# Performance work log

Hardware: AMD Instinct MI355X
Metric: run time of the kernel (lower is better)

The kernel has to match this reference:

```python
import jax, jax.numpy as jnp
import numpy as np

N = 100_000   # nodes
E = 1_250_000 # edges
D = 64        # node feature dim
H = 64        # hidden_channels
C = 10        # num_classes
G = 128       # graphs in batch


def setup_inputs() -> dict:
    key = jax.random.key(0)
    ks = jax.random.split(key, 12)
    x = jax.random.normal(ks[0], (N, D), dtype=jnp.float32)
    edge_index = jax.random.randint(ks[1], (2, E), 0, N, dtype=jnp.int64)
    batch = jnp.sort(jax.random.randint(ks[2], (N,), 0, G, dtype=jnp.int64))
    s = lambda fan_in: 1.0 / np.sqrt(fan_in)
    W1 = jax.random.normal(ks[3], (D, H), dtype=jnp.float32) * s(D)
    b1 = jnp.zeros((H,), dtype=jnp.float32)
    W2 = jax.random.normal(ks[4], (H, H), dtype=jnp.float32) * s(H)
    b2 = jnp.zeros((H,), dtype=jnp.float32)
    W3 = jax.random.normal(ks[5], (H, H), dtype=jnp.float32) * s(H)
    b3 = jnp.zeros((H,), dtype=jnp.float32)
    Wl = jax.random.normal(ks[6], (H, C), dtype=jnp.float32) * s(H)
    bl = jnp.zeros((C,), dtype=jnp.float32)
    return {"x": x, "edge_index": edge_index, "batch": batch,
            "W1": W1, "b1": b1, "W2": W2, "b2": b2,
            "W3": W3, "b3": b3, "Wl": Wl, "bl": bl}


def _gcn_conv(h, W, b, src, dst, norm, n_nodes):
    # GCNConv: out[i] = sum_{e: dst(e)=i} norm_e * (h @ W)[src(e)] + b
    h = h @ W
    msg = h[src] * norm[:, None]                       # [E+N, H]
    return jax.ops.segment_sum(msg, dst, num_segments=n_nodes) + b


def reference(x, edge_index, batch, W1, b1, W2, b2, W3, b3, Wl, bl):
    x = x.astype(jnp.float32)
    ei = edge_index.astype(jnp.int64)
    # add self-loops (as PyG gcn_norm does by default)
    loop = jnp.arange(N, dtype=ei.dtype)
    src = jnp.concatenate([ei[0], loop])
    dst = jnp.concatenate([ei[1], loop])
    # symmetric normalization: deg over targets (in-degree incl. self-loops)
    deg = jax.ops.segment_sum(jnp.ones_like(src, dtype=jnp.float32), dst,
                              num_segments=N)
    dinv = jnp.where(deg > 0, jax.lax.rsqrt(jnp.maximum(deg, 1.0)), 0.0)
    norm = dinv[src] * dinv[dst]                       # [E+N]

    h = jax.nn.relu(_gcn_conv(x, W1, b1, src, dst, norm, N))
    h = jax.nn.relu(_gcn_conv(h, W2, b2, src, dst, norm, N))
    h = _gcn_conv(h, W3, b3, src, dst, norm, N)

    # global_mean_pool over graph ids
    ones = jnp.ones((N,), dtype=jnp.float32)
    counts = jax.ops.segment_sum(ones, batch, num_segments=G)
    sums = jax.ops.segment_sum(h, batch, num_segments=G)
    pooled = sums / jnp.maximum(counts, 1.0)[:, None]  # [G, H]

    # dropout is identity in eval mode
    return pooled @ Wl + bl                            # [G, C]
```

## Files before the change

### kernel.cpp

```cpp
#include <hip/hip_runtime.h>
#include <hip/hip_bf16.h>


#define BSHIFT 7
#define BNODES (1 << BSHIFT)
#define EPB    8192
#define MAXDEG 8192
#define MAXBUCKET 32768

typedef __attribute__((ext_vector_type(8))) short bf16x8;
typedef __attribute__((ext_vector_type(4))) float f32x4;

__device__ __forceinline__ void atomAddF(float* p, float v) {
#if defined(__gfx90a__) || defined(__gfx940__) || defined(__gfx941__) || defined(__gfx942__) || defined(__gfx950__)
    unsafeAtomicAdd(p, v);
#else
    atomicAdd(p, v);
#endif
}

__device__ __forceinline__ unsigned short f2bf(float x) {
    unsigned u = __float_as_uint(x);
    u += 0x7FFFu + ((u >> 16) & 1u);
    return (unsigned short)(u >> 16);
}
__device__ __forceinline__ float bf2f(unsigned short b) {
    return __uint_as_float((unsigned)b << 16);
}

__global__ __launch_bounds__(256)
void k_bhist(const int* __restrict__ dst, int* __restrict__ cnt_all,
             int nE, int nBuckets) {
    __shared__ int cnt[1024];
    const int t = threadIdx.x;
    const int blk = blockIdx.x * EPB;
    for (int b = t; b < nBuckets; b += 256) cnt[b] = 0;
    __syncthreads();
#pragma unroll 4
    for (int i = 0; i < EPB / 256; i++) {
        int e = blk + i * 256 + t;
        if (e < nE) atomicAdd(&cnt[dst[e] >> BSHIFT], 1);
    }
    __syncthreads();
    for (int b = t; b < nBuckets; b += 256)
        cnt_all[(size_t)blockIdx.x * nBuckets + b] = cnt[b];
}

__global__ __launch_bounds__(256)
void k_colscan(int* __restrict__ cnt_all, int* __restrict__ bcnt,
               int nBlocks, int nBuckets) {
    int b = blockIdx.x * blockDim.x + threadIdx.x;
    if (b >= nBuckets) return;
    int running = 0;
    for (int blk = 0; blk < nBlocks; blk++) {
        size_t idx = (size_t)blk * nBuckets + b;
        int v = cnt_all[idx];
        cnt_all[idx] = running;
        running += v;
    }
    bcnt[b] = running;
}

__global__ void k_bscan(const int* __restrict__ bcnt, int* __restrict__ bbase,
                        int nb, int nE) {
    __shared__ int s[256];
    const int t = threadIdx.x;
    const int base = t * 4;
    int v0 = (base + 0 < nb) ? bcnt[base + 0] : 0;
    int v1 = (base + 1 < nb) ? bcnt[base + 1] : 0;
    int v2 = (base + 2 < nb) ? bcnt[base + 2] : 0;
    int v3 = (base + 3 < nb) ? bcnt[base + 3] : 0;
    int tsum = v0 + v1 + v2 + v3;
    s[t] = tsum;
    __syncthreads();
    for (int off = 1; off < 256; off <<= 1) {
        int val = 0;
        if (t >= off) val = s[t - off];
        __syncthreads();
        if (t >= off) s[t] += val;
        __syncthreads();
    }
    int excl = s[t] - tsum;
    if (base + 0 < nb) bbase[base + 0] = excl;
    if (base + 1 < nb) bbase[base + 1] = excl + v0;
    if (base + 2 < nb) bbase[base + 2] = excl + v0 + v1;
    if (base + 3 < nb) bbase[base + 3] = excl + v0 + v1 + v2;
    if (t == 0) bbase[nb] = nE;
}

__global__ __launch_bounds__(256)
void k_bucket(const int* __restrict__ src, const int* __restrict__ dst,
              const int* __restrict__ bbase, const int* __restrict__ cnt_all,
              int* __restrict__ staging, int nE, int nBuckets) {
    __shared__ int cnt[1024];
    __shared__ int lbase[1024];
    const int t = threadIdx.x;
    const int blk = blockIdx.x * EPB;

    for (int b = t; b < nBuckets; b += 256) {
        lbase[b] = bbase[b] + cnt_all[(size_t)blockIdx.x * nBuckets + b];
        cnt[b] = 0;
    }
    __syncthreads();
#pragma unroll 4
    for (int i = 0; i < EPB / 256; i++) {
        int e = blk + i * 256 + t;
        if (e < nE) {
            int s0 = src[e], d0 = dst[e];
            int b = d0 >> BSHIFT;
            int off = atomicAdd(&cnt[b], 1);
            int pos = lbase[b] + off;
            if ((unsigned)pos < (unsigned)nE)
                staging[pos] = (s0 << BSHIFT) | (d0 & (BNODES - 1));
        }
    }
}

__global__ __launch_bounds__(256)
void k_sort(const int* __restrict__ staging, const int* __restrict__ bbase,
            int* __restrict__ csr_s, int* __restrict__ rowptr,
            int* __restrict__ rowend, float* __restrict__ dinv,
            int n, int nE) {
    __shared__ int c[BNODES];
    __shared__ int sc[BNODES];
    __shared__ int cur[BNODES];
    const int t = threadIdx.x;
    const int b = blockIdx.x;
    const int node0 = b << BSHIFT;

    int seg0 = bbase[b];
    int seg1 = bbase[b + 1];
    seg0 = max(0, min(seg0, nE));
    seg1 = max(seg0, min(seg1, nE));
    seg1 = min(seg1, seg0 + MAXBUCKET);

    if (t < BNODES) c[t] = 0;
    __syncthreads();
    for (int e = seg0 + t; e < seg1; e += 256)
        atomicAdd(&c[staging[e] & (BNODES - 1)], 1);
    __syncthreads();
    if (t < BNODES) sc[t] = c[t];
    __syncthreads();
    for (int off = 1; off < BNODES; off <<= 1) {
        int v = 0;
        if (t >= off && t < BNODES) v = sc[t - off];
        __syncthreads();
        if (t >= off && t < BNODES) sc[t] += v;
        __syncthreads();
    }
    if (t < BNODES) {
        int excl = sc[t] - c[t];
        cur[t] = excl;
        int node = node0 + t;
        if (node < n) {
            rowptr[node] = seg0 + excl;
            rowend[node] = seg0 + excl + c[t];
            dinv[node]   = rsqrtf((float)c[t] + 1.0f);
        }
    }
    __syncthreads();
    for (int e = seg0 + t; e < seg1; e += 256) {
        int p = staging[e];
        int l = p & (BNODES - 1);
        int pos = seg0 + atomicAdd(&cur[l], 1);
        if ((unsigned)pos < (unsigned)nE)
            csr_s[pos] = ((unsigned)p) >> BSHIFT;
    }
}

__global__ __launch_bounds__(256)
void k_wfill(const int* __restrict__ csr_s, const float* __restrict__ dinv,
             float* __restrict__ csr_w, int nE, int n) {
    int e = blockIdx.x * blockDim.x + threadIdx.x;
    if (e < nE) {
        int s = csr_s[e];
        s = max(0, min(s, n - 1));
        csr_w[e] = dinv[s];
    }
}

__global__ void k_wprep(const float* __restrict__ W1, const float* __restrict__ W2,
                        const float* __restrict__ W3, unsigned short* __restrict__ Wt) {
    const float* W = (blockIdx.x == 0) ? W1 : ((blockIdx.x == 1) ? W2 : W3);
    unsigned short* o = Wt + blockIdx.x * 4096;
    for (int idx = threadIdx.x; idx < 4096; idx += 256) {
        int h = idx >> 6, k = idx & 63;
        o[idx] = f2bf(W[k * 64 + h]);
    }
}

template<bool RELU, typename AT>
__global__ __launch_bounds__(256)
void k_gemm(const AT* __restrict__ in, const unsigned short* __restrict__ Wt,
            const float* __restrict__ bias, unsigned short* __restrict__ out, int n) {
    const int lane = threadIdx.x & 63;
    const int wid  = threadIdx.x >> 6;
    const int col  = lane & 15;
    const int quad = lane >> 4;
    const int node0w = blockIdx.x * 64 + wid * 16;
    const int nodeA  = node0w + col;
    const bool validA = nodeA < n;

    f32x4 zero4 = {0.f, 0.f, 0.f, 0.f};
    f32x4 acc0 = zero4, acc1 = zero4, acc2 = zero4, acc3 = zero4;

#pragma unroll
    for (int ks = 0; ks < 64; ks += 32) {
        const int kb = ks + quad * 8;
        float a[8];
        if constexpr (sizeof(AT) == 4) {
            float4 a0 = make_float4(0.f, 0.f, 0.f, 0.f);
            float4 a1 = make_float4(0.f, 0.f, 0.f, 0.f);
            if (validA) {
                a0 = *(const float4*)((const float*)in + (size_t)nodeA * 64 + kb);
                a1 = *(const float4*)((const float*)in + (size_t)nodeA * 64 + kb + 4);
            }
            a[0] = a0.x; a[1] = a0.y; a[2] = a0.z; a[3] = a0.w;
            a[4] = a1.x; a[5] = a1.y; a[6] = a1.z; a[7] = a1.w;
        } else {
            ushort4 h0 = make_ushort4(0, 0, 0, 0), h1 = make_ushort4(0, 0, 0, 0);
            if (validA) {
                h0 = *(const ushort4*)((const unsigned short*)in + (size_t)nodeA * 64 + kb);
                h1 = *(const ushort4*)((const unsigned short*)in + (size_t)nodeA * 64 + kb + 4);
            }
            a[0] = bf2f(h0.x); a[1] = bf2f(h0.y); a[2] = bf2f(h0.z); a[3] = bf2f(h0.w);
            a[4] = bf2f(h1.x); a[5] = bf2f(h1.y); a[6] = bf2f(h1.z); a[7] = bf2f(h1.w);
        }
        if (RELU) {
#pragma unroll
            for (int i = 0; i < 8; i++) a[i] = fmaxf(a[i] + bias[kb + i], 0.f);
        }
        bf16x8 af;
#pragma unroll
        for (int i = 0; i < 8; i++) af[i] = (short)f2bf(a[i]);

        const bf16x8 b0f = *(const bf16x8*)(Wt + ((0 * 16 + col) * 64 + kb));
        const bf16x8 b1f = *(const bf16x8*)(Wt + ((1 * 16 + col) * 64 + kb));
        const bf16x8 b2f = *(const bf16x8*)(Wt + ((2 * 16 + col) * 64 + kb));
        const bf16x8 b3f = *(const bf16x8*)(Wt + ((3 * 16 + col) * 64 + kb));
        acc0 = __builtin_amdgcn_mfma_f32_16x16x32_bf16(af, b0f, acc0, 0, 0, 0);
        acc1 = __builtin_amdgcn_mfma_f32_16x16x32_bf16(af, b1f, acc1, 0, 0, 0);
        acc2 = __builtin_amdgcn_mfma_f32_16x16x32_bf16(af, b2f, acc2, 0, 0, 0);
        acc3 = __builtin_amdgcn_mfma_f32_16x16x32_bf16(af, b3f, acc3, 0, 0, 0);
    }

#pragma unroll
    for (int r = 0; r < 4; r++) {
        int nn = node0w + quad * 4 + r;
        if (nn < n) {
            size_t base = (size_t)nn * 64 + col;
            out[base +  0] = f2bf(acc0[r]);
            out[base + 16] = f2bf(acc1[r]);
            out[base + 32] = f2bf(acc2[r]);
            out[base + 48] = f2bf(acc3[r]);
        }
    }
}

template<int LAYER>
__global__ __launch_bounds__(256)
void k_agg(const unsigned short* __restrict__ hW, const int* __restrict__ rowptr,
           const int* __restrict__ rowend, const int* __restrict__ csr_s,
           const float* __restrict__ csr_w, const float* __restrict__ dinv,
           unsigned short* __restrict__ aggb, int n, int nE) {
    const int lane = threadIdx.x & 63;
    const int node = blockIdx.x * 4 + (threadIdx.x >> 6);
    if (node >= n) return;
    int row = rowptr[node];
    int end = rowend[node];
    row = max(0, min(row, nE));
    end = max(row, min(end, nE));
    end = min(end, row + MAXDEG);
    const float di = dinv[node];
    float acc0 = di * di * bf2f(hW[(size_t)node * 64 + lane]);
    float acc1 = 0.f, acc2 = 0.f, acc3 = 0.f;

    for (int base = row; base < end; base += 64) {
        const int m = min(64, end - base);
        int   s_l = 0;
        float w_l = 0.f;
        if (base + lane < end) {
            s_l = csr_s[base + lane];
            w_l = csr_w[base + lane] * di;
        }
        int j = 0;
        for (; j + 8 <= m; j += 8) {
            int   s0 = __shfl(s_l, j),     s1 = __shfl(s_l, j + 1);
            int   s2 = __shfl(s_l, j + 2), s3 = __shfl(s_l, j + 3);
            int   s4 = __shfl(s_l, j + 4), s5 = __shfl(s_l, j + 5);
            int   s6 = __shfl(s_l, j + 6), s7 = __shfl(s_l, j + 7);
            float w0 = __shfl(w_l, j),     w1 = __shfl(w_l, j + 1);
            float w2 = __shfl(w_l, j + 2), w3 = __shfl(w_l, j + 3);
            float w4 = __shfl(w_l, j + 4), w5 = __shfl(w_l, j + 5);
            float w6 = __shfl(w_l, j + 6), w7 = __shfl(w_l, j + 7);
            float h0 = bf2f(hW[(size_t)s0 * 64 + lane]);
            float h1 = bf2f(hW[(size_t)s1 * 64 + lane]);
            float h2 = bf2f(hW[(size_t)s2 * 64 + lane]);
            float h3 = bf2f(hW[(size_t)s3 * 64 + lane]);
            float h4 = bf2f(hW[(size_t)s4 * 64 + lane]);
            float h5 = bf2f(hW[(size_t)s5 * 64 + lane]);
            float h6 = bf2f(hW[(size_t)s6 * 64 + lane]);
            float h7 = bf2f(hW[(size_t)s7 * 64 + lane]);
            acc0 += w0 * h0 + w4 * h4;
            acc1 += w1 * h1 + w5 * h5;
            acc2 += w2 * h2 + w6 * h6;
            acc3 += w3 * h3 + w7 * h7;
        }
        for (; j + 2 <= m; j += 2) {
            int   s0 = __shfl(s_l, j),  s1 = __shfl(s_l, j + 1);
            float w0 = __shfl(w_l, j),  w1 = __shfl(w_l, j + 1);
            acc0 += w0 * bf2f(hW[(size_t)s0 * 64 + lane]);
            acc1 += w1 * bf2f(hW[(size_t)s1 * 64 + lane]);
        }
        for (; j < m; j++) {
            int   sj = __shfl(s_l, j);
            float wj = __shfl(w_l, j);
            acc0 += wj * bf2f(hW[(size_t)sj * 64 + lane]);
        }
    }
    aggb[(size_t)node * 64 + lane] = f2bf((acc0 + acc1) + (acc2 + acc3));
}


__global__ void k_pool(const unsigned short* __restrict__ aggb,
                       const int* __restrict__ batch,
                       float* __restrict__ pool, float* __restrict__ cnt, int n) {
    const int lane = threadIdx.x;
    const int base = blockIdx.x * 64;
    int g_cur = -1, run = 0;
    float acc = 0.f;
    for (int j = 0; j < 64; j++) {
        int node = base + j;
        if (node >= n) break;
        int g = batch[node];
        if (g != g_cur) {
            if (g_cur >= 0) {
                atomAddF(&pool[g_cur * 64 + lane], acc);
                if (lane == 0) atomAddF(&cnt[g_cur], (float)run);
            }
            g_cur = g; acc = 0.f; run = 0;
        }
        acc += bf2f(aggb[(size_t)node * 64 + lane]);
        run++;
    }
    if (g_cur >= 0) {
        atomAddF(&pool[g_cur * 64 + lane], acc);
        if (lane == 0) atomAddF(&cnt[g_cur], (float)run);
    }
}

__global__ void k_final(const float* __restrict__ pool, const float* __restrict__ cnt,
                        const float* __restrict__ b3, const float* __restrict__ Wl,
                        const float* __restrict__ bl, float* __restrict__ out) {
    __shared__ float s[64];
    const int g = blockIdx.x, t = threadIdx.x;
    float c = fmaxf(cnt[g], 1.0f);
    s[t] = pool[g * 64 + t] / c + b3[t];
    __syncthreads();
    if (t < 10) {
        float acc = bl[t];
#pragma unroll
        for (int k = 0; k < 64; k++) acc += s[k] * Wl[k * 10 + t];
        out[g * 10 + t] = acc;
    }
}

extern "C" void kernel_launch(void* const* d_in, const int* in_sizes, int n_in,
                              void* d_out, int out_size, void* d_ws, size_t ws_size,
                              hipStream_t stream) {
    const float* x   = (const float*)d_in[0];
    const int*   ei  = (const int*)d_in[1];
    const int*   bat = (const int*)d_in[2];
    const float* W1  = (const float*)d_in[3];
    const float* b1  = (const float*)d_in[4];
    const float* W2  = (const float*)d_in[5];
    const float* b2  = (const float*)d_in[6];
    const float* W3  = (const float*)d_in[7];
    const float* b3  = (const float*)d_in[8];
    const float* Wl  = (const float*)d_in[9];
    const float* bl  = (const float*)d_in[10];
    float* out = (float*)d_out;

    const int N_ = in_sizes[0] / 64;
    const int E_ = in_sizes[1] / 2;
    const int G_ = out_size / 10;
    const int NB_ = (N_ + BNODES - 1) >> BSHIFT;
    const int bin_blocks = (E_ + EPB - 1) / EPB;

    char* p = (char*)d_ws;
    int*   staging = (int*)p;   p += (size_t)E_ * 4;
    int*   csr_s  = (int*)p;    p += (size_t)E_ * 4;
    float* csr_w  = (float*)p;  p += (size_t)E_ * 4;
    unsigned short* aggb = (unsigned short*)p; p += (size_t)N_ * 64 * 2;
    unsigned short* hW   = (unsigned short*)p; p += (size_t)N_ * 64 * 2;
    float* dinv   = (float*)p;  p += (size_t)N_ * 4;
    int*   rowptr = (int*)p;    p += (size_t)N_ * 4;
    int*   rowend = (int*)p;    p += (size_t)N_ * 4;
    float* pool   = (float*)p;  p += (size_t)G_ * 64 * 4;
    float* cnt    = (float*)p;  p += (size_t)G_ * 4;
    unsigned short* Wt = (unsigned short*)p; p += 3 * 4096 * 2;
    int*   bcnt   = (int*)p;    p += (size_t)(NB_ + 1) * 4;
    int*   bbase  = (int*)p;    p += (size_t)(NB_ + 1) * 4;
    int*   cnt_all = (int*)p;   p += (size_t)bin_blocks * NB_ * 4;

    const int* srcp = ei;
    const int* dstp = ei + E_;

    hipMemsetAsync(pool, 0, (size_t)(G_ * 64 + G_) * 4, stream);

    k_wprep<<<3, 256, 0, stream>>>(W1, W2, W3, Wt);
    k_bhist<<<bin_blocks, 256, 0, stream>>>(dstp, cnt_all, E_, NB_);
    k_colscan<<<(NB_ + 255) / 256, 256, 0, stream>>>(cnt_all, bcnt, bin_blocks, NB_);
    k_bscan<<<1, 256, 0, stream>>>(bcnt, bbase, NB_, E_);
    k_bucket<<<bin_blocks, 256, 0, stream>>>(srcp, dstp, bbase, cnt_all,
                                             staging, E_, NB_);
    k_sort<<<NB_, 256, 0, stream>>>(staging, bbase, csr_s, rowptr, rowend,
                                    dinv, N_, E_);
    k_wfill<<<(E_ + 255) / 256, 256, 0, stream>>>(csr_s, dinv, csr_w, E_, N_);

    const int gemm_blocks = (N_ + 63) / 64;
    const int agg_blocks  = (N_ + 3) / 4;

    k_gemm<false, float><<<gemm_blocks, 256, 0, stream>>>(x, Wt, nullptr, hW, N_);
    k_agg<1><<<agg_blocks, 256, 0, stream>>>(hW, rowptr, rowend, csr_s, csr_w,
                                             dinv, aggb, N_, E_);
    k_gemm<true, unsigned short><<<gemm_blocks, 256, 0, stream>>>(aggb, Wt + 4096,
                                                                  b1, hW, N_);
    k_agg<2><<<agg_blocks, 256, 0, stream>>>(hW, rowptr, rowend, csr_s, csr_w,
                                             dinv, aggb, N_, E_);
    k_gemm<true, unsigned short><<<gemm_blocks, 256, 0, stream>>>(aggb, Wt + 8192,
                                                                  b2, hW, N_);
    k_agg<3><<<agg_blocks, 256, 0, stream>>>(hW, rowptr, rowend, csr_s, csr_w,
                                             dinv, aggb, N_, E_);

    k_pool<<<(N_ + 63) / 64, 64, 0, stream>>>(aggb, bat, pool, cnt, N_);
    k_final<<<G_, 64, 0, stream>>>(pool, cnt, b3, Wl, bl, out);
}
```

Baseline: 392.2 us.

## Process two nodes per wavefront in aggregation, parallelize column scan, fuse weight prep

The aggregation kernel now assigns two destination nodes to each wavefront, with half the lanes loading edge indices for each node. This keeps more independent gathers in flight and packs short (~13-edge) rows into one 64-lane chunk. The column scan switches from one serial thread per bucket to one wavefront per bucket doing a shuffle prefix scan. The weight-prep kernel is folded into the histogram launch as extra blocks to save a launch. The cost is divergence when the two nodes' degrees differ, and a smaller unroll depth per node.

```diff
diff --git a/kernel.cpp b/kernel.cpp
--- a/kernel.cpp
+++ b/kernel.cpp
@@ -30,7 +30,19 @@
 
 __global__ __launch_bounds__(256)
 void k_bhist(const int* __restrict__ dst, int* __restrict__ cnt_all,
-             int nE, int nBuckets) {
+             int nE, int nBuckets, int binBlocks,
+             const float* __restrict__ W1, const float* __restrict__ W2,
+             const float* __restrict__ W3, unsigned short* __restrict__ Wt) {
+    if (blockIdx.x >= binBlocks) {
+        int li = blockIdx.x - binBlocks;
+        const float* W = (li == 0) ? W1 : ((li == 1) ? W2 : W3);
+        unsigned short* o = Wt + li * 4096;
+        for (int idx = threadIdx.x; idx < 4096; idx += 256) {
+            int h = idx >> 6, k = idx & 63;
+            o[idx] = f2bf(W[k * 64 + h]);
+        }
+        return;
+    }
     __shared__ int cnt[1024];
     const int t = threadIdx.x;
     const int blk = blockIdx.x * EPB;
@@ -49,16 +61,23 @@
 __global__ __launch_bounds__(256)
 void k_colscan(int* __restrict__ cnt_all, int* __restrict__ bcnt,
                int nBlocks, int nBuckets) {
-    int b = blockIdx.x * blockDim.x + threadIdx.x;
+    const int lane = threadIdx.x & 63;
+    const int b = blockIdx.x * 4 + (threadIdx.x >> 6);
     if (b >= nBuckets) return;
     int running = 0;
-    for (int blk = 0; blk < nBlocks; blk++) {
-        size_t idx = (size_t)blk * nBuckets + b;
-        int v = cnt_all[idx];
-        cnt_all[idx] = running;
-        running += v;
-    }
-    bcnt[b] = running;
+    for (int c = 0; c < nBlocks; c += 64) {
+        int blk = c + lane;
+        int v = (blk < nBlocks) ? cnt_all[(size_t)blk * nBuckets + b] : 0;
+        int incl = v;
+#pragma unroll
+        for (int off = 1; off < 64; off <<= 1) {
+            int tv = __shfl_up(incl, off);
+            if (lane >= off) incl += tv;
+        }
+        if (blk < nBlocks) cnt_all[(size_t)blk * nBuckets + b] = running + (incl - v);
+        running += __shfl(incl, 63);
+    }
+    if (lane == 0) bcnt[b] = running;
 }
 
 __global__ void k_bscan(const int* __restrict__ bcnt, int* __restrict__ bbase,
@@ -176,16 +195,6 @@
         int s = csr_s[e];
         s = max(0, min(s, n - 1));
         csr_w[e] = dinv[s];
-    }
-}
-
-__global__ void k_wprep(const float* __restrict__ W1, const float* __restrict__ W2,
-                        const float* __restrict__ W3, unsigned short* __restrict__ Wt) {
-    const float* W = (blockIdx.x == 0) ? W1 : ((blockIdx.x == 1) ? W2 : W3);
-    unsigned short* o = Wt + blockIdx.x * 4096;
-    for (int idx = threadIdx.x; idx < 4096; idx += 256) {
-        int h = idx >> 6, k = idx & 63;
-        o[idx] = f2bf(W[k * 64 + h]);
     }
 }
 
@@ -264,61 +273,86 @@
            const float* __restrict__ csr_w, const float* __restrict__ dinv,
            unsigned short* __restrict__ aggb, int n, int nE) {
     const int lane = threadIdx.x & 63;
-    const int node = blockIdx.x * 4 + (threadIdx.x >> 6);
-    if (node >= n) return;
-    int row = rowptr[node];
-    int end = rowend[node];
-    row = max(0, min(row, nE));
-    end = max(row, min(end, nE));
-    end = min(end, row + MAXDEG);
-    const float di = dinv[node];
-    float acc0 = di * di * bf2f(hW[(size_t)node * 64 + lane]);
-    float acc1 = 0.f, acc2 = 0.f, acc3 = 0.f;
-
-    for (int base = row; base < end; base += 64) {
-        const int m = min(64, end - base);
+    const int wid  = threadIdx.x >> 6;
+    const int nA = blockIdx.x * 8 + wid * 2;
+    const int nB = nA + 1;
+    if (nA >= n) return;
+    const bool vB = (nB < n);
+
+    int rowA = rowptr[nA], endA = rowend[nA];
+    rowA = max(0, min(rowA, nE)); endA = max(rowA, min(endA, nE));
+    endA = min(endA, rowA + MAXDEG);
+    int rowB = 0, endB = 0;
+    if (vB) {
+        rowB = rowptr[nB]; endB = rowend[nB];
+        rowB = max(0, min(rowB, nE)); endB = max(rowB, min(endB, nE));
+        endB = min(endB, rowB + MAXDEG);
+    }
+    const float diA = dinv[nA];
+    const float diB = vB ? dinv[nB] : 0.f;
+
+    float a0 = diA * diA * bf2f(hW[(size_t)nA * 64 + lane]);
+    float a1 = 0.f, a2 = 0.f, a3 = 0.f;
+    float b0 = vB ? diB * diB * bf2f(hW[(size_t)nB * 64 + lane]) : 0.f;
+    float b1 = 0.f, b2 = 0.f, b3 = 0.f;
+
+    int baseA = rowA, baseB = rowB;
+    while (baseA < endA || baseB < endB) {
+        int mA = max(0, min(32, endA - baseA));
+        int mB = max(0, min(32, endB - baseB));
         int   s_l = 0;
         float w_l = 0.f;
-        if (base + lane < end) {
-            s_l = csr_s[base + lane];
-            w_l = csr_w[base + lane] * di;
-        }
+        if (lane < 32) {
+            if (lane < mA) {
+                int e = baseA + lane;
+                s_l = csr_s[e];
+                w_l = csr_w[e] * diA;
+            }
+        } else {
+            int l2 = lane - 32;
+            if (l2 < mB) {
+                int e = baseB + l2;
+                s_l = csr_s[e];
+                w_l = csr_w[e] * diB;
+            }
+        }
+        const int m = max(mA, mB);
         int j = 0;
-        for (; j + 8 <= m; j += 8) {
-            int   s0 = __shfl(s_l, j),     s1 = __shfl(s_l, j + 1);
-            int   s2 = __shfl(s_l, j + 2), s3 = __shfl(s_l, j + 3);
-            int   s4 = __shfl(s_l, j + 4), s5 = __shfl(s_l, j + 5);
-            int   s6 = __shfl(s_l, j + 6), s7 = __shfl(s_l, j + 7);
-            float w0 = __shfl(w_l, j),     w1 = __shfl(w_l, j + 1);
-            float w2 = __shfl(w_l, j + 2), w3 = __shfl(w_l, j + 3);
-            float w4 = __shfl(w_l, j + 4), w5 = __shfl(w_l, j + 5);
-            float w6 = __shfl(w_l, j + 6), w7 = __shfl(w_l, j + 7);
-            float h0 = bf2f(hW[(size_t)s0 * 64 + lane]);
-            float h1 = bf2f(hW[(size_t)s1 * 64 + lane]);
-            float h2 = bf2f(hW[(size_t)s2 * 64 + lane]);
-            float h3 = bf2f(hW[(size_t)s3 * 64 + lane]);
-            float h4 = bf2f(hW[(size_t)s4 * 64 + lane]);
-            float h5 = bf2f(hW[(size_t)s5 * 64 + lane]);
-            float h6 = bf2f(hW[(size_t)s6 * 64 + lane]);
-            float h7 = bf2f(hW[(size_t)s7 * 64 + lane]);
-            acc0 += w0 * h0 + w4 * h4;
-            acc1 += w1 * h1 + w5 * h5;
-            acc2 += w2 * h2 + w6 * h6;
-            acc3 += w3 * h3 + w7 * h7;
-        }
-        for (; j + 2 <= m; j += 2) {
-            int   s0 = __shfl(s_l, j),  s1 = __shfl(s_l, j + 1);
-            float w0 = __shfl(w_l, j),  w1 = __shfl(w_l, j + 1);
-            acc0 += w0 * bf2f(hW[(size_t)s0 * 64 + lane]);
-            acc1 += w1 * bf2f(hW[(size_t)s1 * 64 + lane]);
+        for (; j + 4 <= m; j += 4) {
+            int   sA0 = __shfl(s_l, j),      sA1 = __shfl(s_l, j + 1);
+            int   sA2 = __shfl(s_l, j + 2),  sA3 = __shfl(s_l, j + 3);
+            int   sB0 = __shfl(s_l, j + 32), sB1 = __shfl(s_l, j + 33);
+            int   sB2 = __shfl(s_l, j + 34), sB3 = __shfl(s_l, j + 35);
+            float wA0 = __shfl(w_l, j),      wA1 = __shfl(w_l, j + 1);
+            float wA2 = __shfl(w_l, j + 2),  wA3 = __shfl(w_l, j + 3);
+            float wB0 = __shfl(w_l, j + 32), wB1 = __shfl(w_l, j + 33);
+            float wB2 = __shfl(w_l, j + 34), wB3 = __shfl(w_l, j + 35);
+            float hA0 = bf2f(hW[(size_t)sA0 * 64 + lane]);
+            float hA1 = bf2f(hW[(size_t)sA1 * 64 + lane]);
+            float hA2 = bf2f(hW[(size_t)sA2 * 64 + lane]);
+            float hA3 = bf2f(hW[(size_t)sA3 * 64 + lane]);
+            float hB0 = bf2f(hW[(size_t)sB0 * 64 + lane]);
+            float hB1 = bf2f(hW[(size_t)sB1 * 64 + lane]);
+            float hB2 = bf2f(hW[(size_t)sB2 * 64 + lane]);
+            float hB3 = bf2f(hW[(size_t)sB3 * 64 + lane]);
+            a0 += wA0 * hA0; a1 += wA1 * hA1;
+            a2 += wA2 * hA2; a3 += wA3 * hA3;
+            b0 += wB0 * hB0; b1 += wB1 * hB1;
+            b2 += wB2 * hB2; b3 += wB3 * hB3;
         }
         for (; j < m; j++) {
-            int   sj = __shfl(s_l, j);
-            float wj = __shfl(w_l, j);
-            acc0 += wj * bf2f(hW[(size_t)sj * 64 + lane]);
-        }
-    }
-    aggb[(size_t)node * 64 + lane] = f2bf((acc0 + acc1) + (acc2 + acc3));
+            int   sA = __shfl(s_l, j);
+            float wA = __shfl(w_l, j);
+            int   sB = __shfl(s_l, j + 32);
+            float wB = __shfl(w_l, j + 32);
+            a0 += wA * bf2f(hW[(size_t)sA * 64 + lane]);
+            b0 += wB * bf2f(hW[(size_t)sB * 64 + lane]);
+        }
+        baseA += mA;
+        baseB += mB;
+    }
+    aggb[(size_t)nA * 64 + lane] = f2bf((a0 + a1) + (a2 + a3));
+    if (vB) aggb[(size_t)nB * 64 + lane] = f2bf((b0 + b1) + (b2 + b3));
 }
 
 
@@ -408,9 +442,9 @@
 
     hipMemsetAsync(pool, 0, (size_t)(G_ * 64 + G_) * 4, stream);
 
-    k_wprep<<<3, 256, 0, stream>>>(W1, W2, W3, Wt);
-    k_bhist<<<bin_blocks, 256, 0, stream>>>(dstp, cnt_all, E_, NB_);
-    k_colscan<<<(NB_ + 255) / 256, 256, 0, stream>>>(cnt_all, bcnt, bin_blocks, NB_);
+    k_bhist<<<bin_blocks + 3, 256, 0, stream>>>(dstp, cnt_all, E_, NB_,
+                                                bin_blocks, W1, W2, W3, Wt);
+    k_colscan<<<(NB_ + 3) / 4, 256, 0, stream>>>(cnt_all, bcnt, bin_blocks, NB_);
     k_bscan<<<1, 256, 0, stream>>>(bcnt, bbase, NB_, E_);
     k_bucket<<<bin_blocks, 256, 0, stream>>>(srcp, dstp, bbase, cnt_all,
                                              staging, E_, NB_);
@@ -419,7 +453,7 @@
     k_wfill<<<(E_ + 255) / 256, 256, 0, stream>>>(csr_s, dinv, csr_w, E_, N_);
 
     const int gemm_blocks = (N_ + 63) / 64;
-    const int agg_blocks  = (N_ + 3) / 4;
+    const int agg_blocks  = (N_ + 7) / 8;
 
     k_gemm<false, float><<<gemm_blocks, 256, 0, stream>>>(x, Wt, nullptr, hW, N_);
     k_agg<1><<<agg_blocks, 256, 0, stream>>>(hW, rowptr, rowend, csr_s, csr_w,
```

Result: faster. 345.8 us (-11.8%).
